# Optimization experiments

Hardware: AMD Instinct MI355X
Metric: run time of the kernel (lower is better)

The kernel has to match this reference:

```python
import jax, jax.numpy as jnp
import numpy as np

NB_EXPERTS = 16
TOP_K = 2


def setup_inputs() -> dict:
    key = jax.random.key(0)
    k1, k2, k3, k4, k5 = jax.random.split(key, 5)
    B, D, E, P = 8192, 768, NB_EXPERTS, 4
    return {
        "h": jax.random.normal(k1, (B, D, E), dtype=jnp.float32),
        "x": jax.random.normal(k2, (B, D), dtype=jnp.float32),
        "expert_weights": jax.random.normal(k3, (E, D), dtype=jnp.float32) * 0.02,
        "bias": jax.random.normal(k4, (E,), dtype=jnp.float32) * 0.02,
        "permutation_weights": jax.random.uniform(k5, (P, E, E), dtype=jnp.float32),
    }


def reference(h, x, expert_weights, bias, permutation_weights):
    # Router logits: [B, E]
    logits = x @ expert_weights.T + bias[None, :]
    # Top-k selection and scatter back to dense [B, E] (non-selected = 0)
    vals, idx = jax.lax.top_k(logits, TOP_K)
    B = logits.shape[0]
    rows = jnp.arange(B)[:, None]                       # [B, 1]
    scattered = jnp.zeros_like(logits).at[rows, idx].set(vals)
    # Mask zeros to -inf, softmax over experts (axis 1)
    masked = jnp.where(scattered == 0.0, -jnp.inf, scattered)
    softmaxes = jax.nn.softmax(masked, axis=1)          # [B, E]
    # Permutation: mean over leading axis, then bik,ij->bjk with k==1
    P_mean = jnp.mean(permutation_weights, axis=0)       # [E, E]
    s_perm = softmaxes @ P_mean                          # [B, E]
    # Weighted combine of expert outputs: [B, D, E] x [B, E] -> [B, D]
    y = jnp.einsum('bde,be->bd', h, s_perm)
    soft_averages = jnp.mean(s_perm, axis=0)[:, None]    # [E, 1]
    hard_averages = jnp.mean((s_perm >= 1e-05).astype(s_perm.dtype), axis=0)[:, None]  # [E, 1]
    return y, soft_averages, hard_averages
```

## Files before the change

### kernel.cpp

```cpp
#include <hip/hip_runtime.h>
#include <math.h>

#define BB 8192
#define DD 768
#define EE 16
#define PP 4
#define ROWS_PER_BLK 16

__global__ __launch_bounds__(256) void gating_kernel(
    const float* __restrict__ x,
    const float* __restrict__ W,
    const float* __restrict__ bias,
    const float* __restrict__ Pw,
    float* __restrict__ sp_ws,
    float* __restrict__ avgs)
{
    __shared__ float Pm[EE * EE];
    __shared__ float aS[EE], aH[EE];

    const int t = threadIdx.x;

    {
        float s = 0.f;
        #pragma unroll
        for (int p = 0; p < PP; ++p) s += Pw[p * EE * EE + t];
        Pm[t] = s * 0.25f;
    }
    if (t < EE) { aS[t] = 0.f; aH[t] = 0.f; }
    __syncthreads();

    const int wave = t >> 6;
    const int lane = t & 63;
    const int r_in = lane >> 4;
    const int e    = lane & 15;
    const int row  = blockIdx.x * ROWS_PER_BLK + wave * 4 + r_in;

    const float4* x4 = (const float4*)(x + (size_t)row * DD);
    const float4* w4 = (const float4*)(W + (size_t)e * DD);
    float4 acc = {0.f, 0.f, 0.f, 0.f};
    #pragma unroll 4
    for (int k = 0; k < DD / 4; ++k) {
        float4 a = x4[k], b = w4[k];
        acc.x = fmaf(a.x, b.x, acc.x);
        acc.y = fmaf(a.y, b.y, acc.y);
        acc.z = fmaf(a.z, b.z, acc.z);
        acc.w = fmaf(a.w, b.w, acc.w);
    }
    const float logit = acc.x + acc.y + acc.z + acc.w + bias[e];

    float v0 = logit; int i0 = e;
    #pragma unroll
    for (int m = 1; m < 16; m <<= 1) {
        float ov = __shfl_xor(v0, m, 16);
        int   oi = __shfl_xor(i0, m, 16);
        if (ov > v0 || (ov == v0 && oi < i0)) { v0 = ov; i0 = oi; }
    }
    float v1 = (e == i0) ? -INFINITY : logit; int i1 = e;
    #pragma unroll
    for (int m = 1; m < 16; m <<= 1) {
        float ov = __shfl_xor(v1, m, 16);
        int   oi = __shfl_xor(i1, m, 16);
        if (ov > v1 || (ov == v1 && oi < i1)) { v1 = ov; i1 = oi; }
    }

    const float z0 = (v0 == 0.f) ? -INFINITY : v0;
    const float z1 = (v1 == 0.f) ? -INFINITY : v1;
    const float mx = fmaxf(z0, z1);
    const float e0 = expf(z0 - mx), e1 = expf(z1 - mx);
    const float inv = 1.f / (e0 + e1);
    const float sm0 = e0 * inv, sm1 = e1 * inv;

    const float s = sm0 * Pm[i0 * EE + e] + sm1 * Pm[i1 * EE + e];
    sp_ws[(size_t)row * EE + e] = s;

    float ssum = s;
    float hsum = (s >= 1e-5f) ? 1.f : 0.f;
    ssum += __shfl_xor(ssum, 16, 64);
    ssum += __shfl_xor(ssum, 32, 64);
    hsum += __shfl_xor(hsum, 16, 64);
    hsum += __shfl_xor(hsum, 32, 64);
    if (lane < 16) {
        atomicAdd(&aS[e], ssum);
        atomicAdd(&aH[e], hsum);
    }
    __syncthreads();
    if (t < EE) {
        const float invB = 1.0f / (float)BB;
        atomicAdd(&avgs[t],      aS[t] * invB);
        atomicAdd(&avgs[EE + t], aH[t] * invB);
    }
}

__global__ __launch_bounds__(256) void combine_kernel(
    const float* __restrict__ h,
    const float* __restrict__ sp_ws,
    float* __restrict__ y)
{
    const int t = threadIdx.x;
    const int b = blockIdx.x;
    const int q = t & 3;

    const float4 s4 = ((const float4*)(sp_ws + (size_t)b * EE))[q];

    const float4* h4 = (const float4*)(h + (size_t)b * DD * EE);
    float* yb = y + (size_t)b * DD;

    #pragma unroll
    for (int it = 0; it < 12; ++it) {
        const int u = it * 256 + t;
        float4 a = h4[u];
        float p = a.x * s4.x + a.y * s4.y + a.z * s4.z + a.w * s4.w;
        p += __shfl_xor(p, 1, 64);
        p += __shfl_xor(p, 2, 64);
        if (q == 0) yb[u >> 2] = p;
    }
}

extern "C" void kernel_launch(void* const* d_in, const int* in_sizes, int n_in,
                              void* d_out, int out_size, void* d_ws, size_t ws_size,
                              hipStream_t stream) {
    const float* h    = (const float*)d_in[0];
    const float* x    = (const float*)d_in[1];
    const float* W    = (const float*)d_in[2];
    const float* bias = (const float*)d_in[3];
    const float* Pw   = (const float*)d_in[4];

    float* y    = (float*)d_out;
    float* avgs = y + (size_t)BB * DD;
    float* sp_ws = (float*)d_ws;

    hipMemsetAsync(avgs, 0, 2 * EE * sizeof(float), stream);

    gating_kernel<<<BB / ROWS_PER_BLK, 256, 0, stream>>>(x, W, bias, Pw, sp_ws, avgs);
    combine_kernel<<<BB, 256, 0, stream>>>(h, sp_ws, y);
}
```

Baseline: 151.8 us.

## Fuse gating and combine kernels into one per-row-block kernel

Merges the router/top-k/softmax gating kernel and the weighted-combine kernel into a single launch. Each wave now computes one row's logits with its K dimension split across four 16-lane segments plus a shuffle reduction, and the permuted softmax weights stay in LDS instead of a global workspace. The goal is to remove the second launch and the workspace round trip, and to let the h streaming overlap with gating across blocks. In exchange there are more blocks, each with more per-block atomics on the averages, and the W reads are repeated for every 4 rows instead of every 16.

```diff
diff --git a/kernel.cpp b/kernel.cpp
--- a/kernel.cpp
+++ b/kernel.cpp
@@ -5,20 +5,27 @@
 #define DD 768
 #define EE 16
 #define PP 4
-#define ROWS_PER_BLK 16
+#define RPB 4
 
-__global__ __launch_bounds__(256) void gating_kernel(
+__global__ __launch_bounds__(256, 4) void moe_fused(
+    const float* __restrict__ h,
     const float* __restrict__ x,
     const float* __restrict__ W,
     const float* __restrict__ bias,
     const float* __restrict__ Pw,
-    float* __restrict__ sp_ws,
+    float* __restrict__ y,
     float* __restrict__ avgs)
 {
     __shared__ float Pm[EE * EE];
+    __shared__ float sp_lds[RPB][EE];
     __shared__ float aS[EE], aH[EE];
 
-    const int t = threadIdx.x;
+    const int t    = threadIdx.x;
+    const int w    = t >> 6;
+    const int lane = t & 63;
+    const int e    = lane & 15;
+    const int seg  = lane >> 4;
+    const int row  = blockIdx.x * RPB + w;
 
     {
         float s = 0.f;
@@ -29,24 +36,22 @@
     if (t < EE) { aS[t] = 0.f; aH[t] = 0.f; }
     __syncthreads();
 
-    const int wave = t >> 6;
-    const int lane = t & 63;
-    const int r_in = lane >> 4;
-    const int e    = lane & 15;
-    const int row  = blockIdx.x * ROWS_PER_BLK + wave * 4 + r_in;
-
     const float4* x4 = (const float4*)(x + (size_t)row * DD);
     const float4* w4 = (const float4*)(W + (size_t)e * DD);
     float4 acc = {0.f, 0.f, 0.f, 0.f};
-    #pragma unroll 4
-    for (int k = 0; k < DD / 4; ++k) {
-        float4 a = x4[k], b = w4[k];
+    #pragma unroll 6
+    for (int i = 0; i < 48; ++i) {
+        const int k4 = seg + 4 * i;
+        float4 a = x4[k4], b = w4[k4];
         acc.x = fmaf(a.x, b.x, acc.x);
         acc.y = fmaf(a.y, b.y, acc.y);
         acc.z = fmaf(a.z, b.z, acc.z);
         acc.w = fmaf(a.w, b.w, acc.w);
     }
-    const float logit = acc.x + acc.y + acc.z + acc.w + bias[e];
+    float part = (acc.x + acc.y) + (acc.z + acc.w);
+    part += __shfl_xor(part, 16, 64);
+    part += __shfl_xor(part, 32, 64);
+    const float logit = part + bias[e];
 
     float v0 = logit; int i0 = e;
     #pragma unroll
@@ -71,48 +76,34 @@
     const float sm0 = e0 * inv, sm1 = e1 * inv;
 
     const float s = sm0 * Pm[i0 * EE + e] + sm1 * Pm[i1 * EE + e];
-    sp_ws[(size_t)row * EE + e] = s;
-
-    float ssum = s;
-    float hsum = (s >= 1e-5f) ? 1.f : 0.f;
-    ssum += __shfl_xor(ssum, 16, 64);
-    ssum += __shfl_xor(ssum, 32, 64);
-    hsum += __shfl_xor(hsum, 16, 64);
-    hsum += __shfl_xor(hsum, 32, 64);
-    if (lane < 16) {
-        atomicAdd(&aS[e], ssum);
-        atomicAdd(&aH[e], hsum);
+    if (seg == 0) {
+        sp_lds[w][e] = s;
+        atomicAdd(&aS[e], s);
+        atomicAdd(&aH[e], (s >= 1e-5f) ? 1.f : 0.f);
     }
     __syncthreads();
+
     if (t < EE) {
         const float invB = 1.0f / (float)BB;
         atomicAdd(&avgs[t],      aS[t] * invB);
         atomicAdd(&avgs[EE + t], aH[t] * invB);
     }
-}
 
-__global__ __launch_bounds__(256) void combine_kernel(
-    const float* __restrict__ h,
-    const float* __restrict__ sp_ws,
-    float* __restrict__ y)
-{
-    const int t = threadIdx.x;
-    const int b = blockIdx.x;
     const int q = t & 3;
-
-    const float4 s4 = ((const float4*)(sp_ws + (size_t)b * EE))[q];
-
-    const float4* h4 = (const float4*)(h + (size_t)b * DD * EE);
-    float* yb = y + (size_t)b * DD;
-
-    #pragma unroll
-    for (int it = 0; it < 12; ++it) {
-        const int u = it * 256 + t;
-        float4 a = h4[u];
-        float p = a.x * s4.x + a.y * s4.y + a.z * s4.z + a.w * s4.w;
-        p += __shfl_xor(p, 1, 64);
-        p += __shfl_xor(p, 2, 64);
-        if (q == 0) yb[u >> 2] = p;
+    for (int r = 0; r < RPB; ++r) {
+        const float4 s4 = ((const float4*)&sp_lds[r][0])[q];
+        const size_t rw = (size_t)(blockIdx.x * RPB + r);
+        const float4* h4 = (const float4*)(h + rw * DD * EE);
+        float* yr = y + rw * DD;
+        #pragma unroll
+        for (int it = 0; it < 12; ++it) {
+            const int u = it * 256 + t;
+            float4 a = h4[u];
+            float p = a.x * s4.x + a.y * s4.y + a.z * s4.z + a.w * s4.w;
+            p += __shfl_xor(p, 1, 64);
+            p += __shfl_xor(p, 2, 64);
+            if (q == 0) yr[u >> 2] = p;
+        }
     }
 }
 
@@ -127,10 +118,8 @@
 
     float* y    = (float*)d_out;
     float* avgs = y + (size_t)BB * DD;
-    float* sp_ws = (float*)d_ws;
 
     hipMemsetAsync(avgs, 0, 2 * EE * sizeof(float), stream);
 
-    gating_kernel<<<BB / ROWS_PER_BLK, 256, 0, stream>>>(x, W, bias, Pw, sp_ws, avgs);
-    combine_kernel<<<BB, 256, 0, stream>>>(h, sp_ws, y);
+    moe_fused<<<BB / RPB, 256, 0, stream>>>(h, x, W, bias, Pw, y, avgs);
 }
```

New measurement: 147.0 us. 3.2% less time.
